# Kernel optimization log

Measured on AMD Instinct MI355X. Metric: run time of the kernel, lower is better.

The kernel has to match this reference:

```python
import jax, jax.numpy as jnp
import numpy as np

K, D, Q, N = 32, 256, 16, 8192


def setup_inputs() -> dict:
    key = jax.random.key(0)
    kx, km, kl = jax.random.split(key, 3)
    X = jax.random.normal(kx, (N, D), dtype=jnp.float32)
    # mirrors MFA.__init__ parameter init
    log_pi = jnp.full((K,), -jnp.log(jnp.float32(K)), dtype=jnp.float32)
    mu = 0.1 * jax.random.normal(km, (K, D), dtype=jnp.float32)
    Lambda = 0.1 * jax.random.normal(kl, (K, D, Q), dtype=jnp.float32)
    log_psi = jnp.full((D,), jnp.log(jnp.float32(0.01)), dtype=jnp.float32)
    return {"X": X, "log_pi": log_pi, "mu": mu, "Lambda": Lambda, "log_psi": log_psi}


def reference(X, log_pi, mu, Lambda, log_psi):
    """Batched-over-K translation of MFA.e_step (full-cov Cholesky log_prob)."""
    psi = jnp.exp(log_psi) + 1e-6                       # [D]
    eye = jnp.eye(D, dtype=X.dtype)
    # C_k = Lambda_k Lambda_k^T + diag(psi) + 1e-5 I    -> [K, D, D]
    C = jnp.einsum('kdq,keq->kde', Lambda, Lambda) + (jnp.diag(psi) + 1e-5 * eye)[None]
    L = jnp.linalg.cholesky(C)                          # [K, D, D]
    diff = X[None, :, :] - mu[:, None, :]               # [K, N, D]
    # whiten: solve L y = (x - mu)^T  -> [K, D, N]
    y = jax.scipy.linalg.solve_triangular(L, jnp.swapaxes(diff, 1, 2), lower=True)
    maha = jnp.sum(y * y, axis=1)                       # [K, N]
    logdet = 2.0 * jnp.sum(jnp.log(jnp.diagonal(L, axis1=1, axis2=2)), axis=1)  # [K]
    log2pi = jnp.log(jnp.asarray(2.0 * np.pi, dtype=X.dtype))
    log_prob = -0.5 * (D * log2pi + logdet[:, None] + maha)  # [K, N]
    log_resps = log_prob.T + log_pi[None, :]            # [N, K]
    log_likelihood = jax.nn.logsumexp(log_resps, axis=1)  # [N]
    log_resp_norm = log_resps - log_likelihood[:, None]
    return log_resp_norm, log_likelihood
```

## Files before the change

kernel.cpp:

```cpp
#include <hip/hip_runtime.h>
#include <math.h>

#define KK 32
#define DD 256
#define QQ 16
#define NN 8192
#define LOG2PI 1.8378770664093453f
#define NCT 36
#define CPW 9

typedef __attribute__((ext_vector_type(8))) short short8v;
typedef __attribute__((ext_vector_type(4))) float float4v;

__device__ __forceinline__ unsigned short f2bf(float f) {
    union { float f; unsigned int u; } v; v.f = f;
    unsigned int u = v.u;
    return (unsigned short)((u + 0x7FFFu + ((u >> 16) & 1u)) >> 16);
}

__global__ __launch_bounds__(256) void mfa_setup_k(
    const float* __restrict__ log_pi,
    const float* __restrict__ mu,
    const float* __restrict__ Lambda,
    const float* __restrict__ log_psi,
    unsigned short* __restrict__ Wb,
    float* __restrict__ constk2,
    float* __restrict__ wvec)
{
    __shared__ float inv_a_s[DD];
    __shared__ float Ls[DD][QQ];
    __shared__ float Lsia[DD][QQ];
    __shared__ float Ms[QQ][QQ + 1];
    __shared__ float Lc[QQ][QQ + 1];
    __shared__ float red_lg[4], red_m2[4], redq[4][QQ];
    __shared__ float sum_log_a_s, mu2a_s, ld_s;

    const int k = blockIdx.x;
    const int tid = threadIdx.x;
    const int wv = tid >> 6;

    const float a = expf(log_psi[tid]) + 1e-6f + 1e-5f;
    const float ia = 1.0f / a;
    inv_a_s[tid] = ia;
    const float mud = mu[k * DD + tid];

    float lg = logf(a);
    float m2 = mud * mud * ia;
    #pragma unroll
    for (int off = 32; off; off >>= 1) {
        lg += __shfl_down(lg, off, 64);
        m2 += __shfl_down(m2, off, 64);
    }
    if ((tid & 63) == 0) { red_lg[wv] = lg; red_m2[wv] = m2; }

    const float* Lk = Lambda + (size_t)k * DD * QQ;
    for (int i = tid; i < DD * QQ; i += 256) Ls[i >> 4][i & 15] = Lk[i];
    __syncthreads();

    #pragma unroll
    for (int q = 0; q < QQ; ++q) Lsia[tid][q] = Ls[tid][q] * ia;
    if (tid == 0) {
        sum_log_a_s = red_lg[0] + red_lg[1] + red_lg[2] + red_lg[3];
        mu2a_s      = red_m2[0] + red_m2[1] + red_m2[2] + red_m2[3];
    }
    __syncthreads();

    {
        const int q1 = tid >> 4, q2 = tid & 15;
        float b = 0.f;
        for (int d = 0; d < DD; ++d) b = fmaf(Lsia[d][q1], Ls[d][q2], b);
        Ms[q1][q2] = b + (q1 == q2 ? 1.0f : 0.0f);
    }
    __syncthreads();

    if (tid < QQ) {
        const int i = tid;
        float mrow[QQ];
        #pragma unroll
        for (int j = 0; j < QQ; ++j) mrow[j] = Ms[i][j];
        float l[QQ];
        float ldiag = 0.f;
        #pragma unroll
        for (int j = 0; j < QQ; ++j) {
            float s = mrow[j];
            #pragma unroll
            for (int t = 0; t < QQ; ++t) {
                if (t < j) s = fmaf(-l[t], __shfl(l[t], j, 64), s);
            }
            const float piv = __shfl(s, j, 64);
            const float ljj = sqrtf(piv);
            const float val = s / ljj;
            l[j] = (i == j) ? ljj : ((i > j) ? val : 0.f);
            if (i == j) ldiag = logf(ljj);
        }
        #pragma unroll
        for (int j = 0; j < QQ; ++j) Lc[i][j] = l[j];
        #pragma unroll
        for (int mask = 1; mask <= 8; mask <<= 1) ldiag += __shfl_xor(ldiag, mask, 64);
        if (i == 0) ld_s = ldiag;
    }
    __syncthreads();

    if (tid == 0) {
        const float logdetC = sum_log_a_s + 2.0f * ld_s;
        constk2[k] = log_pi[k] - 0.5f * ((float)DD * LOG2PI + logdetC + mu2a_s);
    }

    float tv[QQ];
    {
        float y[QQ];
        #pragma unroll
        for (int q = 0; q < QQ; ++q) {
            float s = Ls[tid][q];
            #pragma unroll
            for (int m = 0; m < QQ; ++m) {
                if (m < q) s = fmaf(-Lc[q][m], y[m], s);
            }
            y[q] = s / Lc[q][q];
        }
        #pragma unroll
        for (int q = 0; q < QQ; ++q) tv[q] = y[q] * ia;
    }

    #pragma unroll
    for (int q = 0; q < QQ; ++q) {
        float v = tv[q] * mud;
        #pragma unroll
        for (int off = 32; off; off >>= 1) v += __shfl_down(v, off, 64);
        if ((tid & 63) == 0) redq[wv][q] = v;
    }
    __syncthreads();
    if (tid < QQ) wvec[k * QQ + tid] = redq[0][tid] + redq[1][tid] + redq[2][tid] + redq[3][tid];

    {
        const int d = tid;
        const int kt = d >> 5, l_hi = (d >> 3) & 3, j = d & 7;
        #pragma unroll
        for (int q = 0; q < QQ; ++q) {
            const size_t idx = (((size_t)(kt * NCT + k) * 64) + l_hi * 16 + q) * 8 + j;
            Wb[idx] = f2bf(tv[q]);
        }
        const size_t idx = (((size_t)(kt * NCT + 32 + (k >> 4)) * 64) + l_hi * 16 + (k & 15)) * 8 + j;
        Wb[idx] = f2bf(mud * ia);
    }
    if (k < 2) {
        for (int i = tid; i < 512; i += 256) {
            const int kt = i >> 6, lane = i & 63;
            const size_t base = ((size_t)(kt * NCT + 34 + k) * 64 + lane) * 8;
            #pragma unroll
            for (int j = 0; j < 8; ++j) Wb[base + j] = 0;
        }
    }
}

__global__ __launch_bounds__(256) void mfa_gemm_fused(
    const float* __restrict__ X,
    const float* __restrict__ log_psi,
    const unsigned short* __restrict__ Wb,
    const float* __restrict__ constk2,
    const float* __restrict__ wvec,
    float* __restrict__ out)
{
    __shared__ short As[8 * 64 * 8];
    __shared__ float inv_a_s[DD];
    __shared__ float w_s[KK][QQ];
    __shared__ float ck_s[KK];
    __shared__ float sx_s[16];
    __shared__ float corr_s[16][KK + 1];
    __shared__ float xmu_s[16][KK + 1];

    const int tid = threadIdx.x;
    const int lane = tid & 63, wv = tid >> 6;
    const int r0 = blockIdx.x * 16;

    inv_a_s[tid] = 1.0f / (expf(log_psi[tid]) + 1e-6f + 1e-5f);
    if (tid < KK) ck_s[tid] = constk2[tid];
    for (int i = tid; i < KK * QQ; i += 256) ((float*)w_s)[i] = wvec[i];

    #pragma unroll
    for (int rep = 0; rep < 2; ++rep) {
        const int c = tid + rep * 256;
        const int kt = c >> 6, lc = c & 63;
        const int m = lc & 15, d0 = kt * 32 + ((lc >> 4) & 3) * 8;
        const float4* xp = (const float4*)(X + (size_t)(r0 + m) * DD + d0);
        const float4 x0 = xp[0], x1 = xp[1];
        short8v av;
        av[0] = (short)f2bf(x0.x); av[1] = (short)f2bf(x0.y);
        av[2] = (short)f2bf(x0.z); av[3] = (short)f2bf(x0.w);
        av[4] = (short)f2bf(x1.x); av[5] = (short)f2bf(x1.y);
        av[6] = (short)f2bf(x1.z); av[7] = (short)f2bf(x1.w);
        *(short8v*)&As[(size_t)(kt * 64 + lc) * 8] = av;
    }
    __syncthreads();

    const int sw = wv * CPW;
    float4v acc[CPW];
    #pragma unroll
    for (int ct = 0; ct < CPW; ++ct)
        #pragma unroll
        for (int r = 0; r < 4; ++r) acc[ct][r] = 0.f;

    #pragma unroll
    for (int kt = 0; kt < 8; ++kt) {
        const short8v a = *(const short8v*)&As[(size_t)(kt * 64 + lane) * 8];
        const short8v* Wp = (const short8v*)Wb + (size_t)(kt * NCT + sw) * 64 + lane;
        #pragma unroll
        for (int ct = 0; ct < CPW; ++ct) {
            const short8v bf = Wp[ct * 64];
            acc[ct] = __builtin_amdgcn_mfma_f32_16x16x32_bf16(a, bf, acc[ct], 0, 0, 0);
        }
    }

    {
        const int n = tid >> 4, part = tid & 15;
        const float4* xp = (const float4*)(X + (size_t)(r0 + n) * DD + part * 16);
        float s = 0.f;
        #pragma unroll
        for (int i = 0; i < 4; ++i) {
            const float4 v = xp[i];
            const int d = part * 16 + i * 4;
            s = fmaf(v.x * inv_a_s[d + 0], v.x, s);
            s = fmaf(v.y * inv_a_s[d + 1], v.y, s);
            s = fmaf(v.z * inv_a_s[d + 2], v.z, s);
            s = fmaf(v.w * inv_a_s[d + 3], v.w, s);
        }
        s += __shfl_xor(s, 1, 64);
        s += __shfl_xor(s, 2, 64);
        s += __shfl_xor(s, 4, 64);
        s += __shfl_xor(s, 8, 64);
        if (part == 0) sx_s[n] = s;
    }

    #pragma unroll
    for (int ct = 0; ct < CPW; ++ct) {
        const int cti = sw + ct;
        if (cti < 32) {
            const float w = w_s[cti][lane & 15];
            float q0 = acc[ct][0] - w, q1 = acc[ct][1] - w,
                  q2 = acc[ct][2] - w, q3 = acc[ct][3] - w;
            q0 *= q0; q1 *= q1; q2 *= q2; q3 *= q3;
            #pragma unroll
            for (int mask = 1; mask <= 8; mask <<= 1) {
                q0 += __shfl_xor(q0, mask, 64);
                q1 += __shfl_xor(q1, mask, 64);
                q2 += __shfl_xor(q2, mask, 64);
                q3 += __shfl_xor(q3, mask, 64);
            }
            if ((lane & 15) == 0) {
                const int nb = (lane >> 4) * 4;
                corr_s[nb + 0][cti] = q0; corr_s[nb + 1][cti] = q1;
                corr_s[nb + 2][cti] = q2; corr_s[nb + 3][cti] = q3;
            }
        } else if (cti < 34) {
            const int kk = (cti - 32) * 16 + (lane & 15);
            const int nb = (lane >> 4) * 4;
            xmu_s[nb + 0][kk] = acc[ct][0]; xmu_s[nb + 1][kk] = acc[ct][1];
            xmu_s[nb + 2][kk] = acc[ct][2]; xmu_s[nb + 3][kk] = acc[ct][3];
        }
    }
    __syncthreads();

    if (tid < 16) {
        const int n = tid;
        const float sxh = 0.5f * sx_s[n];
        float lp[KK];
        float m = -INFINITY;
        #pragma unroll
        for (int k = 0; k < KK; ++k) {
            const float v = ck_s[k] - sxh + xmu_s[n][k] + 0.5f * corr_s[n][k];
            lp[k] = v;
            m = fmaxf(m, v);
        }
        float sum = 0.f;
        #pragma unroll
        for (int k = 0; k < KK; ++k) sum += expf(lp[k] - m);
        const float lse = m + logf(sum);
        float4* o = (float4*)(out + (size_t)(r0 + n) * KK);
        #pragma unroll
        for (int k4 = 0; k4 < KK / 4; ++k4)
            o[k4] = make_float4(lp[4 * k4 + 0] - lse, lp[4 * k4 + 1] - lse,
                                lp[4 * k4 + 2] - lse, lp[4 * k4 + 3] - lse);
        out[(size_t)NN * KK + r0 + n] = lse;
    }
}

extern "C" void kernel_launch(void* const* d_in, const int* in_sizes, int n_in,
                              void* d_out, int out_size, void* d_ws, size_t ws_size,
                              hipStream_t stream) {
    const float* X       = (const float*)d_in[0];
    const float* log_pi  = (const float*)d_in[1];
    const float* mu      = (const float*)d_in[2];
    const float* Lambda  = (const float*)d_in[3];
    const float* log_psi = (const float*)d_in[4];
    float* out = (float*)d_out;

    unsigned short* Wb = (unsigned short*)d_ws;
    float* constk2 = (float*)((char*)d_ws + 294912);
    float* wvec    = constk2 + KK;

    mfa_setup_k<<<KK, 256, 0, stream>>>(log_pi, mu, Lambda, log_psi, Wb, constk2, wvec);
    mfa_gemm_fused<<<NN / 16, 256, 0, stream>>>(X, log_psi, Wb, constk2, wvec, out);
}
```

Measured before the change: 93.04 us.

## Process 32 rows per block with 8 waves sharing column tiles

Result: slower. 96.13 us (+3.3%).

```diff
diff --git a/kernel.cpp b/kernel.cpp
--- a/kernel.cpp
+++ b/kernel.cpp
@@ -153,7 +153,7 @@
     }
 }
 
-__global__ __launch_bounds__(256) void mfa_gemm_fused(
+__global__ __launch_bounds__(512, 2) void mfa_gemm_fused(
     const float* __restrict__ X,
     const float* __restrict__ log_psi,
     const unsigned short* __restrict__ Wb,
@@ -161,55 +161,24 @@
     const float* __restrict__ wvec,
     float* __restrict__ out)
 {
-    __shared__ short As[8 * 64 * 8];
+    __shared__ short As[16 * 64 * 8];
     __shared__ float inv_a_s[DD];
     __shared__ float w_s[KK][QQ];
     __shared__ float ck_s[KK];
-    __shared__ float sx_s[16];
-    __shared__ float corr_s[16][KK + 1];
-    __shared__ float xmu_s[16][KK + 1];
+    __shared__ float sx_s[32];
+    __shared__ float corr_s[32][KK + 1];
+    __shared__ float xmu_s[32][KK + 1];
 
     const int tid = threadIdx.x;
     const int lane = tid & 63, wv = tid >> 6;
-    const int r0 = blockIdx.x * 16;
-
-    inv_a_s[tid] = 1.0f / (expf(log_psi[tid]) + 1e-6f + 1e-5f);
+    const int rt = wv & 1;
+    const int sw = (wv >> 1) * CPW;
+    const int r0 = blockIdx.x * 32;
+
+    if (tid < DD) inv_a_s[tid] = 1.0f / (expf(log_psi[tid]) + 1e-6f + 1e-5f);
     if (tid < KK) ck_s[tid] = constk2[tid];
-    for (int i = tid; i < KK * QQ; i += 256) ((float*)w_s)[i] = wvec[i];
-
-    #pragma unroll
-    for (int rep = 0; rep < 2; ++rep) {
-        const int c = tid + rep * 256;
-        const int kt = c >> 6, lc = c & 63;
-        const int m = lc & 15, d0 = kt * 32 + ((lc >> 4) & 3) * 8;
-        const float4* xp = (const float4*)(X + (size_t)(r0 + m) * DD + d0);
-        const float4 x0 = xp[0], x1 = xp[1];
-        short8v av;
-        av[0] = (short)f2bf(x0.x); av[1] = (short)f2bf(x0.y);
-        av[2] = (short)f2bf(x0.z); av[3] = (short)f2bf(x0.w);
-        av[4] = (short)f2bf(x1.x); av[5] = (short)f2bf(x1.y);
-        av[6] = (short)f2bf(x1.z); av[7] = (short)f2bf(x1.w);
-        *(short8v*)&As[(size_t)(kt * 64 + lc) * 8] = av;
-    }
-    __syncthreads();
-
-    const int sw = wv * CPW;
-    float4v acc[CPW];
-    #pragma unroll
-    for (int ct = 0; ct < CPW; ++ct)
-        #pragma unroll
-        for (int r = 0; r < 4; ++r) acc[ct][r] = 0.f;
-
-    #pragma unroll
-    for (int kt = 0; kt < 8; ++kt) {
-        const short8v a = *(const short8v*)&As[(size_t)(kt * 64 + lane) * 8];
-        const short8v* Wp = (const short8v*)Wb + (size_t)(kt * NCT + sw) * 64 + lane;
-        #pragma unroll
-        for (int ct = 0; ct < CPW; ++ct) {
-            const short8v bf = Wp[ct * 64];
-            acc[ct] = __builtin_amdgcn_mfma_f32_16x16x32_bf16(a, bf, acc[ct], 0, 0, 0);
-        }
-    }
+    if (tid < KK * QQ) ((float*)w_s)[tid] = wvec[tid];
+    __syncthreads();
 
     {
         const int n = tid >> 4, part = tid & 15;
@@ -229,6 +198,43 @@
         s += __shfl_xor(s, 4, 64);
         s += __shfl_xor(s, 8, 64);
         if (part == 0) sx_s[n] = s;
+    }
+
+    #pragma unroll
+    for (int rep = 0; rep < 2; ++rep) {
+        const int c = tid + rep * 512;
+        const int g = c >> 6;
+        const int kt = g >> 1, rts = g & 1, lc = c & 63;
+        const int row = r0 + rts * 16 + (lc & 15);
+        const int d0 = kt * 32 + ((lc >> 4) & 3) * 8;
+        const float4* xp = (const float4*)(X + (size_t)row * DD + d0);
+        const float4 x0 = xp[0], x1 = xp[1];
+        short8v av;
+        av[0] = (short)f2bf(x0.x); av[1] = (short)f2bf(x0.y);
+        av[2] = (short)f2bf(x0.z); av[3] = (short)f2bf(x0.w);
+        av[4] = (short)f2bf(x1.x); av[5] = (short)f2bf(x1.y);
+        av[6] = (short)f2bf(x1.z); av[7] = (short)f2bf(x1.w);
+        *(short8v*)&As[(size_t)(g * 64 + lc) * 8] = av;
+    }
+    __syncthreads();
+
+    float4v acc[CPW];
+    #pragma unroll
+    for (int ct = 0; ct < CPW; ++ct)
+        #pragma unroll
+        for (int r = 0; r < 4; ++r) acc[ct][r] = 0.f;
+
+    const short8v* Asv = (const short8v*)As;
+    const short8v* WpL = (const short8v*)Wb + lane;
+
+    #pragma unroll
+    for (int kt = 0; kt < 8; ++kt) {
+        const short8v a = Asv[(kt * 2 + rt) * 64 + lane];
+        #pragma unroll
+        for (int ct = 0; ct < CPW; ++ct) {
+            const short8v bf = WpL[(size_t)(kt * NCT + sw + ct) * 64];
+            acc[ct] = __builtin_amdgcn_mfma_f32_16x16x32_bf16(a, bf, acc[ct], 0, 0, 0);
+        }
     }
 
     #pragma unroll
@@ -247,20 +253,20 @@
                 q3 += __shfl_xor(q3, mask, 64);
             }
             if ((lane & 15) == 0) {
-                const int nb = (lane >> 4) * 4;
+                const int nb = rt * 16 + (lane >> 4) * 4;
                 corr_s[nb + 0][cti] = q0; corr_s[nb + 1][cti] = q1;
                 corr_s[nb + 2][cti] = q2; corr_s[nb + 3][cti] = q3;
             }
         } else if (cti < 34) {
-            const int kk = (cti - 32) * 16 + (lane & 15);
-            const int nb = (lane >> 4) * 4;
-            xmu_s[nb + 0][kk] = acc[ct][0]; xmu_s[nb + 1][kk] = acc[ct][1];
-            xmu_s[nb + 2][kk] = acc[ct][2]; xmu_s[nb + 3][kk] = acc[ct][3];
-        }
-    }
-    __syncthreads();
-
-    if (tid < 16) {
+            const int kk2 = (cti - 32) * 16 + (lane & 15);
+            const int nb = rt * 16 + (lane >> 4) * 4;
+            xmu_s[nb + 0][kk2] = acc[ct][0]; xmu_s[nb + 1][kk2] = acc[ct][1];
+            xmu_s[nb + 2][kk2] = acc[ct][2]; xmu_s[nb + 3][kk2] = acc[ct][3];
+        }
+    }
+    __syncthreads();
+
+    if (tid < 32) {
         const int n = tid;
         const float sxh = 0.5f * sx_s[n];
         float lp[KK];
@@ -299,5 +305,5 @@
     float* wvec    = constk2 + KK;
 
     mfa_setup_k<<<KK, 256, 0, stream>>>(log_pi, mu, Lambda, log_psi, Wb, constk2, wvec);
-    mfa_gemm_fused<<<NN / 16, 256, 0, stream>>>(X, log_psi, Wb, constk2, wvec, out);
+    mfa_gemm_fused<<<NN / 32, 512, 0, stream>>>(X, log_psi, Wb, constk2, wvec, out);
 }
```
